# Performance work log

Measured on AMD Instinct MI355X. Metric: run time of the kernel, lower is better.

The kernel has to match this reference:

```python
import jax, jax.numpy as jnp
import numpy as np

INPUT_SIZE = 256
N_DIM = 128
BATCH = 1024


def setup_inputs() -> dict:
    key = jax.random.key(0)
    ks = jax.random.split(key, 8)
    X = jax.random.normal(ks[0], (BATCH, INPUT_SIZE), dtype=jnp.float32)
    h = jax.random.normal(ks[1], (BATCH, INPUT_SIZE * N_DIM), dtype=jnp.float32)
    W_r = jax.random.normal(ks[2], (INPUT_SIZE, 1, N_DIM), dtype=jnp.float32)
    W_z = jax.random.normal(ks[3], (INPUT_SIZE, 1, N_DIM), dtype=jnp.float32)
    W_h = jax.random.normal(ks[4], (INPUT_SIZE, 1, N_DIM), dtype=jnp.float32)
    # orthogonal init for U (matches nn.init.orthogonal_ in spirit)
    def ortho(k):
        a = jax.random.normal(k, (INPUT_SIZE, N_DIM, N_DIM), dtype=jnp.float32)
        q, _ = jnp.linalg.qr(a)
        return q.astype(jnp.float32)
    U_r = ortho(ks[5])
    U_z = ortho(ks[6])
    U_h = ortho(ks[7])
    b_r = jnp.zeros((INPUT_SIZE, N_DIM), dtype=jnp.float32)
    b_z = jnp.zeros((INPUT_SIZE, N_DIM), dtype=jnp.float32)
    b_h = jnp.zeros((INPUT_SIZE, N_DIM), dtype=jnp.float32)
    return {"X": X, "h": h, "W_r": W_r, "W_z": W_z, "W_h": W_h,
            "U_r": U_r, "U_z": U_z, "U_h": U_h,
            "b_r": b_r, "b_z": b_z, "b_h": b_h}


def reference(X, h, W_r, W_z, W_h, U_r, U_z, U_h, b_r, b_z, b_h):
    B = X.shape[0]
    hg = h.reshape(B, INPUT_SIZE, N_DIM)  # [B, I, D]
    # X contribution: X[b,i] * W[i,0,k] -> [B, I, D]
    xW_r = X[:, :, None] * W_r[:, 0, :][None]
    xW_z = X[:, :, None] * W_z[:, 0, :][None]
    xW_h = X[:, :, None] * W_h[:, 0, :][None]
    # grouped GEMMs: [B,I,D] x [I,D,D] -> [B,I,D]
    r = jax.nn.sigmoid(xW_r + jnp.einsum('bij,ijk->bik', hg, U_r) + b_r)
    z = jax.nn.sigmoid(xW_z + jnp.einsum('bij,ijk->bik', hg, U_z) + b_z)
    h_tilde = jnp.tanh(xW_h + jnp.einsum('bij,ijk->bik', r * hg, U_h) + b_h)
    h_new = z * hg + (1.0 - z) * h_tilde
    return (h_new.reshape(B, INPUT_SIZE * N_DIM),
            h_tilde.reshape(B, INPUT_SIZE * N_DIM))
```

## Files before the change

kernel.cpp:

```cpp
#include <hip/hip_runtime.h>
#include <hip/hip_bf16.h>
#include <stdint.h>

#define I_SIZE 256
#define D_DIM 128
#define BATCH 1024

typedef __attribute__((ext_vector_type(8))) short short8;
typedef __attribute__((ext_vector_type(4))) short short4v;
typedef __attribute__((ext_vector_type(4))) float floatx4;

__device__ inline short f2bf(float f) {
    union { float f; uint32_t u; } v; v.f = f;
    uint32_t u = v.u;
    uint32_t r = (u + 0x7FFFu + ((u >> 16) & 1u)) >> 16;
    return (short)(r & 0xFFFFu);
}
__device__ inline float bf2f(short s) {
    union { uint32_t u; float f; } v; v.u = ((uint32_t)(uint16_t)s) << 16;
    return v.f;
}
__device__ inline uint32_t pkbf(float a, float b) {
    __hip_bfloat162 h = __float22bfloat162_rn(make_float2(a, b));
    union { __hip_bfloat162 h; uint32_t u; } v; v.h = h; return v.u;
}
__device__ inline float sigmoidf_fast(float x) { return 1.0f / (1.0f + __expf(-x)); }
__device__ inline float tanhf_fast(float x)    { return 2.0f / (1.0f + __expf(-2.0f * x)) - 1.0f; }

__global__ __launch_bounds__(256) void transpose_u(
    const float* __restrict__ Ur, const float* __restrict__ Uz,
    const float* __restrict__ Uh, short* __restrict__ ws)
{
    __shared__ short tile[D_DIM * D_DIM];
    const int grp = blockIdx.x;
    const int g   = blockIdx.y;
    const float* Ug = ((g == 0) ? Ur : (g == 1) ? Uz : Uh) + (size_t)grp * (D_DIM * D_DIM);
    const int t = threadIdx.x;
    const int lane = t & 63;
    const int w = t >> 6;

    for (int m = 0; m < 16; ++m) {
        int j0 = w + 4 * (m >> 1);
        int k  = lane + 64 * (m & 1);
        float a0 = Ug[(4 * j0 + 0) * D_DIM + k];
        float a1 = Ug[(4 * j0 + 1) * D_DIM + k];
        float a2 = Ug[(4 * j0 + 2) * D_DIM + k];
        float a3 = Ug[(4 * j0 + 3) * D_DIM + k];
        short4v s; s.x = f2bf(a0); s.y = f2bf(a1); s.z = f2bf(a2); s.w = f2bf(a3);
        int p = (j0 >> 1) ^ (k & 7);
        *(short4v*)&tile[k * D_DIM + p * 8 + 4 * (j0 & 1)] = s;
    }
    __syncthreads();
    short* dst = ws + ((size_t)g * I_SIZE + grp) * (D_DIM * D_DIM);
    for (int q = 0; q < 8; ++q) {
        int off = q * 2048 + t * 8;
        *(short8*)(dst + off) = *(const short8*)&tile[off];
    }
}

#define S_H 136

__global__ __launch_bounds__(1024, 4) void gru_main(
    const float* __restrict__ X, const float* __restrict__ H,
    const float* __restrict__ Wr, const float* __restrict__ Wz, const float* __restrict__ Wh,
    const float* __restrict__ br, const float* __restrict__ bz, const float* __restrict__ bh,
    const short* __restrict__ Utg, float* __restrict__ out)
{
    __shared__ short Ut[3 * D_DIM * D_DIM];
    __shared__ short hgb[D_DIM * S_H];
    __shared__ float Wl[6][D_DIM];

    const int tid   = threadIdx.x;
    const int group = blockIdx.x;
    const int lane  = tid & 63;
    const int w     = tid >> 6;

    if (tid < D_DIM) {
        Wl[0][tid] = Wr[group * D_DIM + tid];
        Wl[1][tid] = Wz[group * D_DIM + tid];
        Wl[2][tid] = Wh[group * D_DIM + tid];
        Wl[3][tid] = br[group * D_DIM + tid];
        Wl[4][tid] = bz[group * D_DIM + tid];
        Wl[5][tid] = bh[group * D_DIM + tid];
    }

    {
        #pragma unroll
        for (int q = 0; q < 6; ++q) {
            int chunk = w * 6 + q;
            int g   = chunk >> 5;
            int off = (chunk & 31) * 1024;
            const char* gp = (const char*)Utg + ((size_t)g * I_SIZE + group) * 32768
                             + off + lane * 16;
            char* lp = ((char*)Ut) + g * 32768 + off;
            __builtin_amdgcn_global_load_lds(
                (const __attribute__((address_space(1))) void*)gp,
                (__attribute__((address_space(3))) void*)lp, 16, 0, 0);
        }
    }
    __syncthreads();

    const int am = lane & 15;
    const int aq = lane >> 4;
    const int rg = w >> 1;
    const int nh = w & 1;
    const int r0 = rg * 16;
    const size_t HOFF = (size_t)BATCH * I_SIZE * D_DIM;
    const int srow = tid >> 3;
    const int scol = (tid & 7) * 4;

    int pswz[4];
    #pragma unroll
    for (int kk = 0; kk < 4; ++kk) pswz[kk] = ((4 * kk + aq) ^ (am & 7)) * 8;

    const floatx4 zero = {0.f, 0.f, 0.f, 0.f};

    for (int pass = 0; pass < 8; ++pass) {
        const int R = pass * 128;

        #pragma unroll
        for (int it = 0; it < 4; ++it) {
            int col = scol + it * 32;
            float4 v = *(const float4*)(H + (size_t)(R + srow) * (I_SIZE * D_DIM)
                                        + group * D_DIM + col);
            uint2 uu; uu.x = pkbf(v.x, v.y); uu.y = pkbf(v.z, v.w);
            *(uint2*)&hgb[srow * S_H + col] = uu;
        }
        __syncthreads();

        short8 a[4];
        #pragma unroll
        for (int kk = 0; kk < 4; ++kk)
            a[kk] = *(const short8*)&hgb[(r0 + am) * S_H + kk * 32 + aq * 8];

        floatx4 accr[4], accz[4];
        #pragma unroll
        for (int t2 = 0; t2 < 4; ++t2) { accr[t2] = zero; accz[t2] = zero; }

        #pragma unroll
        for (int t2 = 0; t2 < 4; ++t2) {
            const int n = nh * 64 + t2 * 16 + am;
            const short* rowp = &Ut[n * D_DIM];
            #pragma unroll
            for (int kk = 0; kk < 4; ++kk)
                accr[t2] = __builtin_amdgcn_mfma_f32_16x16x32_bf16(
                    a[kk], *(const short8*)(rowp + pswz[kk]), accr[t2], 0, 0, 0);
            #pragma unroll
            for (int kk = 0; kk < 4; ++kk)
                accz[t2] = __builtin_amdgcn_mfma_f32_16x16x32_bf16(
                    a[kk], *(const short8*)(rowp + 16384 + pswz[kk]), accz[t2], 0, 0, 0);
        }

        float Xv[4];
        #pragma unroll
        for (int pp = 0; pp < 4; ++pp)
            Xv[pp] = X[(size_t)(R + r0 + aq * 4 + pp) * I_SIZE + group];

        float zr[4][4], hgc[4][4];
        #pragma unroll
        for (int t2 = 0; t2 < 4; ++t2) {
            const int c = nh * 64 + t2 * 16 + am;
            const float wr = Wl[0][c], wz = Wl[1][c], brv = Wl[3][c], bzv = Wl[4][c];
            #pragma unroll
            for (int pp = 0; pp < 4; ++pp) {
                const int rl = r0 + aq * 4 + pp;
                float hgv = bf2f(hgb[rl * S_H + c]);
                float rv = sigmoidf_fast(accr[t2][pp] + Xv[pp] * wr + brv);
                float zv = sigmoidf_fast(accz[t2][pp] + Xv[pp] * wz + bzv);
                zr[t2][pp]  = zv;
                hgc[t2][pp] = hgv;
                hgb[rl * S_H + c] = f2bf(rv * hgv);
            }
        }
        __syncthreads();

        short8 ap[4];
        #pragma unroll
        for (int kk = 0; kk < 4; ++kk)
            ap[kk] = *(const short8*)&hgb[(r0 + am) * S_H + kk * 32 + aq * 8];

        floatx4 acch[4];
        #pragma unroll
        for (int t2 = 0; t2 < 4; ++t2) acch[t2] = zero;
        #pragma unroll
        for (int t2 = 0; t2 < 4; ++t2) {
            const int n = nh * 64 + t2 * 16 + am;
            const short* rowp = &Ut[32768 + n * D_DIM];
            #pragma unroll
            for (int kk = 0; kk < 4; ++kk)
                acch[t2] = __builtin_amdgcn_mfma_f32_16x16x32_bf16(
                    a[0] , *(const short8*)(rowp + pswz[kk]), acch[t2], 0, 0, 0);
        }
        #pragma unroll
        for (int t2 = 0; t2 < 4; ++t2) acch[t2] = zero;
        #pragma unroll
        for (int t2 = 0; t2 < 4; ++t2) {
            const int n = nh * 64 + t2 * 16 + am;
            const short* rowp = &Ut[32768 + n * D_DIM];
            #pragma unroll
            for (int kk = 0; kk < 4; ++kk)
                acch[t2] = __builtin_amdgcn_mfma_f32_16x16x32_bf16(
                    ap[kk], *(const short8*)(rowp + pswz[kk]), acch[t2], 0, 0, 0);
        }

        #pragma unroll
        for (int t2 = 0; t2 < 4; ++t2) {
            const int c = nh * 64 + t2 * 16 + am;
            const float wh = Wl[2][c], bhv = Wl[5][c];
            #pragma unroll
            for (int pp = 0; pp < 4; ++pp) {
                const int rl = r0 + aq * 4 + pp;
                float ht = tanhf_fast(acch[t2][pp] + Xv[pp] * wh + bhv);
                float zv = zr[t2][pp];
                float hn = zv * hgc[t2][pp] + (1.0f - zv) * ht;
                size_t o = (size_t)(R + rl) * (I_SIZE * D_DIM) + group * D_DIM + c;
                out[o]        = hn;
                out[HOFF + o] = ht;
            }
        }
        __syncthreads();
    }
}

#define S_LDS 136
#define THREADS 512
#define CHUNKS 2
#define ROWS_PER_CHUNK (BATCH / CHUNKS)
#define ROWS_PER_PASS 128
#define PASSES (ROWS_PER_CHUNK / ROWS_PER_PASS)

__global__ __launch_bounds__(THREADS, 2) void gru_kernel(
    const float* __restrict__ X, const float* __restrict__ H,
    const float* __restrict__ Wr, const float* __restrict__ Wz, const float* __restrict__ Wh,
    const float* __restrict__ Ur, const float* __restrict__ Uz, const float* __restrict__ Uh,
    const float* __restrict__ br, const float* __restrict__ bz, const float* __restrict__ bh,
    float* __restrict__ out)
{
    __shared__ short Ut[3][D_DIM * S_LDS];
    __shared__ short hgb[ROWS_PER_PASS * S_LDS];
    __shared__ float Wl[6][D_DIM];

    const int tid   = threadIdx.x;
    const int group = blockIdx.x & 255;
    const int chunk = blockIdx.x >> 8;
    const int batch0 = chunk * ROWS_PER_CHUNK;

    if (tid < D_DIM) {
        Wl[0][tid] = Wr[group * D_DIM + tid];
        Wl[1][tid] = Wz[group * D_DIM + tid];
        Wl[2][tid] = Wh[group * D_DIM + tid];
        Wl[3][tid] = br[group * D_DIM + tid];
        Wl[4][tid] = bz[group * D_DIM + tid];
        Wl[5][tid] = bh[group * D_DIM + tid];
    }
    {
        const int jj = tid >> 5;
        const int k0 = (tid & 31) * 4;
        const float* Us0 = Ur + (size_t)group * (D_DIM * D_DIM);
        const float* Us1 = Uz + (size_t)group * (D_DIM * D_DIM);
        const float* Us2 = Uh + (size_t)group * (D_DIM * D_DIM);
        #pragma unroll
        for (int g = 0; g < 3; ++g) {
            const float* Ug = (g == 0) ? Us0 : (g == 1) ? Us1 : Us2;
            for (int rep = 0; rep < 8; ++rep) {
                int j = rep * 16 + jj;
                float4 v = *(const float4*)(Ug + j * D_DIM + k0);
                Ut[g][(k0 + 0) * S_LDS + j] = f2bf(v.x);
                Ut[g][(k0 + 1) * S_LDS + j] = f2bf(v.y);
                Ut[g][(k0 + 2) * S_LDS + j] = f2bf(v.z);
                Ut[g][(k0 + 3) * S_LDS + j] = f2bf(v.w);
            }
        }
    }
    __syncthreads();

    const int lane = tid & 63;
    const int wave = tid >> 6;
    const int am   = lane & 15;
    const int aq   = lane >> 4;
    const int r0   = wave * 16;
    const size_t HOFF = (size_t)BATCH * I_SIZE * D_DIM;

    for (int pass = 0; pass < PASSES; ++pass) {
        const int R = batch0 + pass * ROWS_PER_PASS;
        {
            const int rowp = lane >> 5;
            const int col4 = (lane & 31) * 4;
            #pragma unroll
            for (int it = 0; it < 8; ++it) {
                int rl = r0 + it * 2 + rowp;
                const float* src = H + (size_t)(R + rl) * (I_SIZE * D_DIM) + group * D_DIM + col4;
                float4 v = *(const float4*)src;
                short4v s;
                s.x = f2bf(v.x); s.y = f2bf(v.y); s.z = f2bf(v.z); s.w = f2bf(v.w);
                *(short4v*)&hgb[rl * S_LDS + col4] = s;
            }
        }
        __syncthreads();

        short8 a[4];
        #pragma unroll
        for (int kk = 0; kk < 4; ++kk)
            a[kk] = *(const short8*)&hgb[(r0 + am) * S_LDS + kk * 32 + aq * 8];

        floatx4 zero = {0.f, 0.f, 0.f, 0.f};
        floatx4 accr[8], accz[8];
        #pragma unroll
        for (int t = 0; t < 8; ++t) { accr[t] = zero; accz[t] = zero; }
        #pragma unroll
        for (int t = 0; t < 8; ++t) {
            const int nbase = (t * 16 + am) * S_LDS + aq * 8;
            #pragma unroll
            for (int kk = 0; kk < 4; ++kk)
                accr[t] = __builtin_amdgcn_mfma_f32_16x16x32_bf16(
                    a[kk], *(const short8*)&Ut[0][nbase + kk * 32], accr[t], 0, 0, 0);
            #pragma unroll
            for (int kk = 0; kk < 4; ++kk)
                accz[t] = __builtin_amdgcn_mfma_f32_16x16x32_bf16(
                    a[kk], *(const short8*)&Ut[1][nbase + kk * 32], accz[t], 0, 0, 0);
        }

        float Xv[4];
        #pragma unroll
        for (int pp = 0; pp < 4; ++pp)
            Xv[pp] = X[(size_t)(R + r0 + aq * 4 + pp) * I_SIZE + group];

        float zr[8][4], hgc[8][4];
        #pragma unroll
        for (int t = 0; t < 8; ++t) {
            const int c = t * 16 + am;
            const float wr = Wl[0][c], wz = Wl[1][c], brv = Wl[3][c], bzv = Wl[4][c];
            #pragma unroll
            for (int pp = 0; pp < 4; ++pp) {
                const int rl = r0 + aq * 4 + pp;
                float hgv = bf2f(hgb[rl * S_LDS + c]);
                float rv = sigmoidf_fast(accr[t][pp] + Xv[pp] * wr + brv);
                float zv = sigmoidf_fast(accz[t][pp] + Xv[pp] * wz + bzv);
                zr[t][pp]  = zv;
                hgc[t][pp] = hgv;
                hgb[rl * S_LDS + c] = f2bf(rv * hgv);
            }
        }
        __syncthreads();

        short8 ap[4];
        #pragma unroll
        for (int kk = 0; kk < 4; ++kk)
            ap[kk] = *(const short8*)&hgb[(r0 + am) * S_LDS + kk * 32 + aq * 8];

        floatx4 acch[8];
        #pragma unroll
        for (int t = 0; t < 8; ++t) acch[t] = zero;
        #pragma unroll
        for (int t = 0; t < 8; ++t) {
            const int nbase = (t * 16 + am) * S_LDS + aq * 8;
            #pragma unroll
            for (int kk = 0; kk < 4; ++kk)
                acch[t] = __builtin_amdgcn_mfma_f32_16x16x32_bf16(
                    ap[kk], *(const short8*)&Ut[2][nbase + kk * 32], acch[t], 0, 0, 0);
        }
        #pragma unroll
        for (int t = 0; t < 8; ++t) {
            const int c = t * 16 + am;
            const float wh = Wl[2][c], bhv = Wl[5][c];
            #pragma unroll
            for (int pp = 0; pp < 4; ++pp) {
                const int rl = r0 + aq * 4 + pp;
                float ht = tanhf_fast(acch[t][pp] + Xv[pp] * wh + bhv);
                float zv = zr[t][pp];
                float hn = zv * hgc[t][pp] + (1.0f - zv) * ht;
                size_t o = (size_t)(R + rl) * (I_SIZE * D_DIM) + group * D_DIM + c;
                out[o]        = hn;
                out[HOFF + o] = ht;
            }
        }
        __syncthreads();
    }
}

extern "C" void kernel_launch(void* const* d_in, const int* in_sizes, int n_in,
                              void* d_out, int out_size, void* d_ws, size_t ws_size,
                              hipStream_t stream) {
    const float* X  = (const float*)d_in[0];
    const float* H  = (const float*)d_in[1];
    const float* Wr = (const float*)d_in[2];
    const float* Wz = (const float*)d_in[3];
    const float* Wh = (const float*)d_in[4];
    const float* Ur = (const float*)d_in[5];
    const float* Uz = (const float*)d_in[6];
    const float* Uh = (const float*)d_in[7];
    const float* br = (const float*)d_in[8];
    const float* bz = (const float*)d_in[9];
    const float* bh = (const float*)d_in[10];

    const size_t need = (size_t)3 * I_SIZE * D_DIM * D_DIM * sizeof(short);
    if (ws_size >= need) {
        transpose_u<<<dim3(I_SIZE, 3), dim3(256), 0, stream>>>(Ur, Uz, Uh, (short*)d_ws);
        gru_main<<<dim3(I_SIZE), dim3(1024), 0, stream>>>(
            X, H, Wr, Wz, Wh, br, bz, bh, (const short*)d_ws, (float*)d_out);
    } else {
        gru_kernel<<<dim3(I_SIZE * CHUNKS), dim3(THREADS), 0, stream>>>(
            X, H, Wr, Wz, Wh, Ur, Uz, Uh, br, bz, bh, (float*)d_out);
    }
}
```

Before: 474.6 us.

## Fuse U transpose into main GRU kernel and drop redundant MFMA pass

The separate transpose_u kernel and its bf16 workspace round trip are removed. Each block of the main kernel now loads its group's fp32 U matrices directly, converts them to bf16 and writes them into swizzled LDS. This saves a kernel launch and the extra global write and read of the transposed weights, at the cost of non-async loads in the kernel prologue. A leftover duplicate MFMA loop for the h̃ GEMM, which computed from a[0] and was then discarded, is deleted, along with the unused fallback kernel.

Measured after the change: 462.2 us. 2.6% less time.

```diff
diff --git a/kernel.cpp b/kernel.cpp
--- a/kernel.cpp
+++ b/kernel.cpp
@@ -27,44 +27,14 @@
 __device__ inline float sigmoidf_fast(float x) { return 1.0f / (1.0f + __expf(-x)); }
 __device__ inline float tanhf_fast(float x)    { return 2.0f / (1.0f + __expf(-2.0f * x)) - 1.0f; }
 
-__global__ __launch_bounds__(256) void transpose_u(
-    const float* __restrict__ Ur, const float* __restrict__ Uz,
-    const float* __restrict__ Uh, short* __restrict__ ws)
-{
-    __shared__ short tile[D_DIM * D_DIM];
-    const int grp = blockIdx.x;
-    const int g   = blockIdx.y;
-    const float* Ug = ((g == 0) ? Ur : (g == 1) ? Uz : Uh) + (size_t)grp * (D_DIM * D_DIM);
-    const int t = threadIdx.x;
-    const int lane = t & 63;
-    const int w = t >> 6;
-
-    for (int m = 0; m < 16; ++m) {
-        int j0 = w + 4 * (m >> 1);
-        int k  = lane + 64 * (m & 1);
-        float a0 = Ug[(4 * j0 + 0) * D_DIM + k];
-        float a1 = Ug[(4 * j0 + 1) * D_DIM + k];
-        float a2 = Ug[(4 * j0 + 2) * D_DIM + k];
-        float a3 = Ug[(4 * j0 + 3) * D_DIM + k];
-        short4v s; s.x = f2bf(a0); s.y = f2bf(a1); s.z = f2bf(a2); s.w = f2bf(a3);
-        int p = (j0 >> 1) ^ (k & 7);
-        *(short4v*)&tile[k * D_DIM + p * 8 + 4 * (j0 & 1)] = s;
-    }
-    __syncthreads();
-    short* dst = ws + ((size_t)g * I_SIZE + grp) * (D_DIM * D_DIM);
-    for (int q = 0; q < 8; ++q) {
-        int off = q * 2048 + t * 8;
-        *(short8*)(dst + off) = *(const short8*)&tile[off];
-    }
-}
-
 #define S_H 136
 
-__global__ __launch_bounds__(1024, 4) void gru_main(
+__global__ __launch_bounds__(1024, 4) void gru_fused(
     const float* __restrict__ X, const float* __restrict__ H,
     const float* __restrict__ Wr, const float* __restrict__ Wz, const float* __restrict__ Wh,
+    const float* __restrict__ Ur, const float* __restrict__ Uz, const float* __restrict__ Uh,
     const float* __restrict__ br, const float* __restrict__ bz, const float* __restrict__ bh,
-    const short* __restrict__ Utg, float* __restrict__ out)
+    float* __restrict__ out)
 {
     __shared__ short Ut[3 * D_DIM * D_DIM];
     __shared__ short hgb[D_DIM * S_H];
@@ -85,20 +55,26 @@
     }
 
     {
-        #pragma unroll
-        for (int q = 0; q < 6; ++q) {
-            int chunk = w * 6 + q;
-            int g   = chunk >> 5;
-            int off = (chunk & 31) * 1024;
-            const char* gp = (const char*)Utg + ((size_t)g * I_SIZE + group) * 32768
-                             + off + lane * 16;
-            char* lp = ((char*)Ut) + g * 32768 + off;
-            __builtin_amdgcn_global_load_lds(
-                (const __attribute__((address_space(1))) void*)gp,
-                (__attribute__((address_space(3))) void*)lp, 16, 0, 0);
+        const int kc = tid & 127;
+        const int jb = tid >> 7;
+        #pragma unroll
+        for (int g = 0; g < 3; ++g) {
+            const float* Ug = ((g == 0) ? Ur : (g == 1) ? Uz : Uh)
+                              + (size_t)group * (D_DIM * D_DIM);
+            short* dst = &Ut[g * (D_DIM * D_DIM)];
+            #pragma unroll
+            for (int m = 0; m < 4; ++m) {
+                const int j0 = m * 8 + jb;
+                float a0 = Ug[(4 * j0 + 0) * D_DIM + kc];
+                float a1 = Ug[(4 * j0 + 1) * D_DIM + kc];
+                float a2 = Ug[(4 * j0 + 2) * D_DIM + kc];
+                float a3 = Ug[(4 * j0 + 3) * D_DIM + kc];
+                short4v s; s.x = f2bf(a0); s.y = f2bf(a1); s.z = f2bf(a2); s.w = f2bf(a3);
+                const int p = (j0 >> 1) ^ (kc & 7);
+                *(short4v*)&dst[kc * D_DIM + p * 8 + 4 * (j0 & 1)] = s;
+            }
         }
     }
-    __syncthreads();
 
     const int am = lane & 15;
     const int aq = lane >> 4;
@@ -189,17 +165,6 @@
             #pragma unroll
             for (int kk = 0; kk < 4; ++kk)
                 acch[t2] = __builtin_amdgcn_mfma_f32_16x16x32_bf16(
-                    a[0] , *(const short8*)(rowp + pswz[kk]), acch[t2], 0, 0, 0);
-        }
-        #pragma unroll
-        for (int t2 = 0; t2 < 4; ++t2) acch[t2] = zero;
-        #pragma unroll
-        for (int t2 = 0; t2 < 4; ++t2) {
-            const int n = nh * 64 + t2 * 16 + am;
-            const short* rowp = &Ut[32768 + n * D_DIM];
-            #pragma unroll
-            for (int kk = 0; kk < 4; ++kk)
-                acch[t2] = __builtin_amdgcn_mfma_f32_16x16x32_bf16(
                     ap[kk], *(const short8*)(rowp + pswz[kk]), acch[t2], 0, 0, 0);
         }
 
@@ -213,162 +178,6 @@
                 float ht = tanhf_fast(acch[t2][pp] + Xv[pp] * wh + bhv);
                 float zv = zr[t2][pp];
                 float hn = zv * hgc[t2][pp] + (1.0f - zv) * ht;
-                size_t o = (size_t)(R + rl) * (I_SIZE * D_DIM) + group * D_DIM + c;
-                out[o]        = hn;
-                out[HOFF + o] = ht;
-            }
-        }
-        __syncthreads();
-    }
-}
-
-#define S_LDS 136
-#define THREADS 512
-#define CHUNKS 2
-#define ROWS_PER_CHUNK (BATCH / CHUNKS)
-#define ROWS_PER_PASS 128
-#define PASSES (ROWS_PER_CHUNK / ROWS_PER_PASS)
-
-__global__ __launch_bounds__(THREADS, 2) void gru_kernel(
-    const float* __restrict__ X, const float* __restrict__ H,
-    const float* __restrict__ Wr, const float* __restrict__ Wz, const float* __restrict__ Wh,
-    const float* __restrict__ Ur, const float* __restrict__ Uz, const float* __restrict__ Uh,
-    const float* __restrict__ br, const float* __restrict__ bz, const float* __restrict__ bh,
-    float* __restrict__ out)
-{
-    __shared__ short Ut[3][D_DIM * S_LDS];
-    __shared__ short hgb[ROWS_PER_PASS * S_LDS];
-    __shared__ float Wl[6][D_DIM];
-
-    const int tid   = threadIdx.x;
-    const int group = blockIdx.x & 255;
-    const int chunk = blockIdx.x >> 8;
-    const int batch0 = chunk * ROWS_PER_CHUNK;
-
-    if (tid < D_DIM) {
-        Wl[0][tid] = Wr[group * D_DIM + tid];
-        Wl[1][tid] = Wz[group * D_DIM + tid];
-        Wl[2][tid] = Wh[group * D_DIM + tid];
-        Wl[3][tid] = br[group * D_DIM + tid];
-        Wl[4][tid] = bz[group * D_DIM + tid];
-        Wl[5][tid] = bh[group * D_DIM + tid];
-    }
-    {
-        const int jj = tid >> 5;
-        const int k0 = (tid & 31) * 4;
-        const float* Us0 = Ur + (size_t)group * (D_DIM * D_DIM);
-        const float* Us1 = Uz + (size_t)group * (D_DIM * D_DIM);
-        const float* Us2 = Uh + (size_t)group * (D_DIM * D_DIM);
-        #pragma unroll
-        for (int g = 0; g < 3; ++g) {
-            const float* Ug = (g == 0) ? Us0 : (g == 1) ? Us1 : Us2;
-            for (int rep = 0; rep < 8; ++rep) {
-                int j = rep * 16 + jj;
-                float4 v = *(const float4*)(Ug + j * D_DIM + k0);
-                Ut[g][(k0 + 0) * S_LDS + j] = f2bf(v.x);
-                Ut[g][(k0 + 1) * S_LDS + j] = f2bf(v.y);
-                Ut[g][(k0 + 2) * S_LDS + j] = f2bf(v.z);
-                Ut[g][(k0 + 3) * S_LDS + j] = f2bf(v.w);
-            }
-        }
-    }
-    __syncthreads();
-
-    const int lane = tid & 63;
-    const int wave = tid >> 6;
-    const int am   = lane & 15;
-    const int aq   = lane >> 4;
-    const int r0   = wave * 16;
-    const size_t HOFF = (size_t)BATCH * I_SIZE * D_DIM;
-
-    for (int pass = 0; pass < PASSES; ++pass) {
-        const int R = batch0 + pass * ROWS_PER_PASS;
-        {
-            const int rowp = lane >> 5;
-            const int col4 = (lane & 31) * 4;
-            #pragma unroll
-            for (int it = 0; it < 8; ++it) {
-                int rl = r0 + it * 2 + rowp;
-                const float* src = H + (size_t)(R + rl) * (I_SIZE * D_DIM) + group * D_DIM + col4;
-                float4 v = *(const float4*)src;
-                short4v s;
-                s.x = f2bf(v.x); s.y = f2bf(v.y); s.z = f2bf(v.z); s.w = f2bf(v.w);
-                *(short4v*)&hgb[rl * S_LDS + col4] = s;
-            }
-        }
-        __syncthreads();
-
-        short8 a[4];
-        #pragma unroll
-        for (int kk = 0; kk < 4; ++kk)
-            a[kk] = *(const short8*)&hgb[(r0 + am) * S_LDS + kk * 32 + aq * 8];
-
-        floatx4 zero = {0.f, 0.f, 0.f, 0.f};
-        floatx4 accr[8], accz[8];
-        #pragma unroll
-        for (int t = 0; t < 8; ++t) { accr[t] = zero; accz[t] = zero; }
-        #pragma unroll
-        for (int t = 0; t < 8; ++t) {
-            const int nbase = (t * 16 + am) * S_LDS + aq * 8;
-            #pragma unroll
-            for (int kk = 0; kk < 4; ++kk)
-                accr[t] = __builtin_amdgcn_mfma_f32_16x16x32_bf16(
-                    a[kk], *(const short8*)&Ut[0][nbase + kk * 32], accr[t], 0, 0, 0);
-            #pragma unroll
-            for (int kk = 0; kk < 4; ++kk)
-                accz[t] = __builtin_amdgcn_mfma_f32_16x16x32_bf16(
-                    a[kk], *(const short8*)&Ut[1][nbase + kk * 32], accz[t], 0, 0, 0);
-        }
-
-        float Xv[4];
-        #pragma unroll
-        for (int pp = 0; pp < 4; ++pp)
-            Xv[pp] = X[(size_t)(R + r0 + aq * 4 + pp) * I_SIZE + group];
-
-        float zr[8][4], hgc[8][4];
-        #pragma unroll
-        for (int t = 0; t < 8; ++t) {
-            const int c = t * 16 + am;
-            const float wr = Wl[0][c], wz = Wl[1][c], brv = Wl[3][c], bzv = Wl[4][c];
-            #pragma unroll
-            for (int pp = 0; pp < 4; ++pp) {
-                const int rl = r0 + aq * 4 + pp;
-                float hgv = bf2f(hgb[rl * S_LDS + c]);
-                float rv = sigmoidf_fast(accr[t][pp] + Xv[pp] * wr + brv);
-                float zv = sigmoidf_fast(accz[t][pp] + Xv[pp] * wz + bzv);
-                zr[t][pp]  = zv;
-                hgc[t][pp] = hgv;
-                hgb[rl * S_LDS + c] = f2bf(rv * hgv);
-            }
-        }
-        __syncthreads();
-
-        short8 ap[4];
-        #pragma unroll
-        for (int kk = 0; kk < 4; ++kk)
-            ap[kk] = *(const short8*)&hgb[(r0 + am) * S_LDS + kk * 32 + aq * 8];
-
-        floatx4 acch[8];
-        #pragma unroll
-        for (int t = 0; t < 8; ++t) acch[t] = zero;
-        #pragma unroll
-        for (int t = 0; t < 8; ++t) {
-            const int nbase = (t * 16 + am) * S_LDS + aq * 8;
-            #pragma unroll
-            for (int kk = 0; kk < 4; ++kk)
-                acch[t] = __builtin_amdgcn_mfma_f32_16x16x32_bf16(
-                    ap[kk], *(const short8*)&Ut[2][nbase + kk * 32], acch[t], 0, 0, 0);
-        }
-        #pragma unroll
-        for (int t = 0; t < 8; ++t) {
-            const int c = t * 16 + am;
-            const float wh = Wl[2][c], bhv = Wl[5][c];
-            #pragma unroll
-            for (int pp = 0; pp < 4; ++pp) {
-                const int rl = r0 + aq * 4 + pp;
-                float ht = tanhf_fast(acch[t][pp] + Xv[pp] * wh + bhv);
-                float zv = zr[t][pp];
-                float hn = zv * hgc[t][pp] + (1.0f - zv) * ht;
                 size_t o = (size_t)(R + rl) * (I_SIZE * D_DIM) + group * D_DIM + c;
                 out[o]        = hn;
                 out[HOFF + o] = ht;
@@ -393,13 +202,8 @@
     const float* bz = (const float*)d_in[9];
     const float* bh = (const float*)d_in[10];
 
-    const size_t need = (size_t)3 * I_SIZE * D_DIM * D_DIM * sizeof(short);
-    if (ws_size >= need) {
-        transpose_u<<<dim3(I_SIZE, 3), dim3(256), 0, stream>>>(Ur, Uz, Uh, (short*)d_ws);
-        gru_main<<<dim3(I_SIZE), dim3(1024), 0, stream>>>(
-            X, H, Wr, Wz, Wh, br, bz, bh, (const short*)d_ws, (float*)d_out);
-    } else {
-        gru_kernel<<<dim3(I_SIZE * CHUNKS), dim3(THREADS), 0, stream>>>(
-            X, H, Wr, Wz, Wh, Ur, Uz, Uh, br, bz, bh, (float*)d_out);
-    }
-}
+    (void)d_ws; (void)ws_size;
+
+    gru_fused<<<dim3(I_SIZE), dim3(1024), 0, stream>>>(
+        X, H, Wr, Wz, Wh, Ur, Uz, Uh, br, bz, bh, (float*)d_out);
+}
```
